# Performance work log

Measured on AMD Instinct MI355X. Metric: run time of the kernel, lower is better.

Reference implementation:

```python
import jax, jax.numpy as jnp
import numpy as np

D_IN = 1024
D_OUT = 1024
B = 4
S = 2048


def setup_inputs() -> dict:
    key = jax.random.key(0)
    kx, kq, kk, kv = jax.random.split(key, 4)
    x = jax.random.normal(kx, (B, S, D_IN), dtype=jnp.float32)
    # Linear weights stored as [d_in, d_out] so projection is x @ W
    sc = 1.0 / np.sqrt(D_IN)
    Wq = jax.random.normal(kq, (D_IN, D_OUT), dtype=jnp.float32) * sc
    Wk = jax.random.normal(kk, (D_IN, D_OUT), dtype=jnp.float32) * sc
    Wv = jax.random.normal(kv, (D_IN, D_OUT), dtype=jnp.float32) * sc
    return {"x": x, "Wq": Wq, "Wk": Wk, "Wv": Wv}


def reference(x, Wq, Wk, Wv):
    # q, k, v: [b, s, d_out]
    q = jnp.einsum("bsd,de->bse", x, Wq)
    k = jnp.einsum("bsd,de->bse", x, Wk)
    v = jnp.einsum("bsd,de->bse", x, Wv)
    s = q.shape[1]
    # raw scores [b, s, s]
    scores = jnp.einsum("bqd,bkd->bqk", q, k)
    # causal mask: disallow key j > query i (see notes re: original mask bug)
    causal = jnp.triu(jnp.ones((s, s), dtype=bool), k=1)
    scores = jnp.where(causal[None, :, :], -jnp.inf, scores)
    scale = 1.0 / jnp.sqrt(jnp.asarray(k.shape[-1], dtype=scores.dtype))
    att_weights = jax.nn.softmax(scores * scale, axis=-1)
    # dropout p=0.0 -> identity
    att_output = jnp.einsum("bqk,bkd->bqd", att_weights, v)
    return att_output, att_weights
```

## Files before the change

### kernel.cpp

```cpp
#include <hip/hip_runtime.h>
#include <stdint.h>

#define DIM 1024
#define SEQ 2048
#define NB 4

typedef unsigned short u16;
typedef __bf16 bf16x8 __attribute__((ext_vector_type(8)));
typedef float floatx4 __attribute__((ext_vector_type(4)));

__device__ __forceinline__ u16 f32_to_bf16(float f) {
  union { float f; unsigned u; } v; v.f = f;
  unsigned r = v.u + 0x7FFFu + ((v.u >> 16) & 1u);
  return (u16)(r >> 16);
}

__device__ __forceinline__ void async16(const void* g, void* l) {
  __builtin_amdgcn_global_load_lds(
      (__attribute__((address_space(1))) unsigned int*)g,
      (__attribute__((address_space(3))) unsigned int*)l, 16, 0, 0);
}

__global__ __launch_bounds__(256) void k_prep(const float* __restrict__ x,
                                              const float* __restrict__ Wq,
                                              const float* __restrict__ Wk,
                                              const float* __restrict__ Wv,
                                              u16* __restrict__ xb,
                                              u16* __restrict__ wt) {
  __shared__ u16 tile[32][33];
  const int bid = blockIdx.x;
  const int tid = threadIdx.x;
  if (bid < 4096) {
    int i = bid * 256 + tid;
    float4 a = ((const float4*)x)[i * 2];
    float4 b = ((const float4*)x)[i * 2 + 1];
    ushort4 o0, o1;
    o0.x = f32_to_bf16(a.x); o0.y = f32_to_bf16(a.y);
    o0.z = f32_to_bf16(a.z); o0.w = f32_to_bf16(a.w);
    o1.x = f32_to_bf16(b.x); o1.y = f32_to_bf16(b.y);
    o1.z = f32_to_bf16(b.z); o1.w = f32_to_bf16(b.w);
    ((ushort4*)xb)[i * 2] = o0;
    ((ushort4*)xb)[i * 2 + 1] = o1;
  } else {
    int t = bid - 4096;
    int z = t >> 10;
    int ti = t & 1023;
    int c0 = (ti & 31) * 32, r0 = (ti >> 5) * 32;
    const float* src = (z == 0) ? Wq : (z == 1) ? Wk : Wv;
    u16* d = wt + (size_t)z * DIM * DIM;
    int tx = tid & 31, ty = tid >> 5;
    #pragma unroll
    for (int dy = 0; dy < 32; dy += 8)
      tile[ty + dy][tx] = f32_to_bf16(src[(size_t)(r0 + ty + dy) * DIM + c0 + tx]);
    __syncthreads();
    #pragma unroll
    for (int dy = 0; dy < 32; dy += 8)
      d[(size_t)(c0 + ty + dy) * DIM + r0 + tx] = tile[tx][ty + dy];
  }
}


#define STG(PG, STBASE, SLOT, H, I, KT)                                        \
  async16((PG) + (size_t)((H) * 128 + (I) * 64) * DIM + (KT) * 64,             \
          (STBASE) + (SLOT) * 16384 + (H) * 8192 + (I) * 4096)

#define PHASE(SLOT, KS, MH, RDB, STGS, SYNC)                                   \
  {                                                                            \
    const int go_ = (KS) ? ga1 : ga0;                                          \
    const u16* pa_ = aRd + (SLOT) * 16384;                                     \
    if (RDB) {                                                                 \
      const u16* pb_ = bRd + (SLOT) * 16384;                                   \
      _Pragma("unroll") for (int n = 0; n < 4; ++n)                            \
          bfr[n] = *(const bf16x8*)(pb_ + n * 1024 + go_);                     \
    }                                                                          \
    _Pragma("unroll") for (int m = 0; m < 4; ++m)                              \
        af[m] = *(const bf16x8*)(pa_ + ((MH) * 4 + m) * 1024 + go_);           \
    STGS                                                                       \
    __builtin_amdgcn_s_barrier();                                              \
    asm volatile("s_waitcnt lgkmcnt(0)");                                      \
    __builtin_amdgcn_s_setprio(1);                                             \
    _Pragma("unroll") for (int m = 0; m < 4; ++m)                              \
        _Pragma("unroll") for (int n = 0; n < 4; ++n)                          \
            acc[(MH) * 4 + m][n] = __builtin_amdgcn_mfma_f32_16x16x32_bf16(    \
                af[m], bfr[n], acc[(MH) * 4 + m][n], 0, 0, 0);                 \
    __builtin_amdgcn_s_setprio(0);                                             \
    SYNC                                                                       \
    __builtin_amdgcn_s_barrier();                                              \
  }

__device__ __forceinline__ void core256(const u16* __restrict__ pga,
                                        const u16* __restrict__ pgb,
                                        const u16* aRd, const u16* bRd,
                                        u16* stA, u16* stB,
                                        int ga0, int ga1,
                                        floatx4 acc[8][4], int NITER) {
  bf16x8 af[4], bfr[4];

  STG(pga, stA, 0, 0, 0, 0); STG(pga, stA, 0, 0, 1, 0);
  STG(pga, stA, 0, 1, 0, 0); STG(pga, stA, 0, 1, 1, 0);
  STG(pgb, stB, 0, 0, 0, 0); STG(pgb, stB, 0, 0, 1, 0);
  STG(pgb, stB, 0, 1, 0, 0); STG(pgb, stB, 0, 1, 1, 0);
  STG(pgb, stB, 1, 0, 0, 1); STG(pgb, stB, 1, 0, 1, 1);
  asm volatile("s_waitcnt vmcnt(2)");
  __builtin_amdgcn_sched_barrier(0);
  __builtin_amdgcn_s_barrier();

  for (int t = 0; t < NITER; ++t) {
    const bool more = (t + 1 < NITER);
    const int kA1 = 2 * t + 1;
    const int kN = 2 * t + 2;
    const int kB1n = 2 * t + 3;

    PHASE(0, 0, 0, 1,
          { STG(pga, stA, 1, 0, 0, kA1); STG(pga, stA, 1, 0, 1, kA1); }, {})
    PHASE(0, 0, 1, 0,
          { STG(pga, stA, 1, 1, 0, kA1); STG(pga, stA, 1, 1, 1, kA1); }, {})
    PHASE(0, 1, 0, 1,
          { STG(pgb, stB, 1, 1, 0, kA1); STG(pgb, stB, 1, 1, 1, kA1); }, {})
    PHASE(0, 1, 1, 0,
          { if (more) { STG(pgb, stB, 0, 0, 0, kN); STG(pgb, stB, 0, 0, 1, kN); } },
          { if (more) { asm volatile("s_waitcnt vmcnt(2)"); }
            else      { asm volatile("s_waitcnt vmcnt(0)"); }
            __builtin_amdgcn_sched_barrier(0); })
    PHASE(1, 0, 0, 1,
          { if (more) { STG(pgb, stB, 0, 1, 0, kN); STG(pgb, stB, 0, 1, 1, kN); } }, {})
    PHASE(1, 0, 1, 0,
          { if (more) { STG(pga, stA, 0, 0, 0, kN); STG(pga, stA, 0, 0, 1, kN); } }, {})
    PHASE(1, 1, 0, 1,
          { if (more) { STG(pga, stA, 0, 1, 0, kN); STG(pga, stA, 0, 1, 1, kN); } }, {})
    PHASE(1, 1, 1, 0,
          { if (more) { STG(pgb, stB, 1, 0, 0, kB1n); STG(pgb, stB, 1, 0, 1, kB1n); } },
          { if (more) { asm volatile("s_waitcnt vmcnt(2)");
                        __builtin_amdgcn_sched_barrier(0); } })
  }

  asm volatile("s_waitcnt vmcnt(0)");
}

__global__ __launch_bounds__(512) void k_proj8(const u16* __restrict__ xb,
                                               const u16* __restrict__ wt,
                                               u16* __restrict__ qk,
                                               u16* __restrict__ vT) {
  __shared__ u16 lds[65536];
  const int wg = ((blockIdx.x & 7) * 48) + (blockIdx.x >> 3);
  const int tid = threadIdx.x;
  const int lane = tid & 63;
  const int wid = tid >> 6;

  const u16 *A, *Bt;
  u16* Cout;
  int ldc;
  if (wg < 256) {
    const int z = wg >> 7;
    const int r = wg & 127;
    const int mt = r >> 2, nt = r & 3;
    A = xb + (size_t)mt * 256 * DIM;
    Bt = wt + (size_t)z * DIM * DIM + (size_t)nt * 256 * DIM;
    Cout = qk + (size_t)z * (NB * SEQ * DIM) + (size_t)mt * 256 * DIM + nt * 256;
    ldc = DIM;
  } else {
    const int r = wg - 256;
    const int mt = r & 3, nt = r >> 2;
    A = wt + (size_t)2 * DIM * DIM + (size_t)mt * 256 * DIM;
    Bt = xb + (size_t)nt * 256 * DIM;
    Cout = vT + (size_t)(nt >> 3) * (DIM * SEQ) + (size_t)mt * 256 * SEQ
              + (nt & 7) * 256;
    ldc = SEQ;
  }

  const int srow = wid * 8 + (lane >> 3);
  const int gsrc = (lane & 7) ^ ((lane >> 3) & 7);
  const u16* pga = A + (size_t)srow * DIM + gsrc * 8;
  const u16* pgb = Bt + (size_t)srow * DIM + gsrc * 8;
  u16* stA = lds + wid * 512;
  u16* stB = lds + 32768 + wid * 512;

  const int wr = wid >> 2, wc = wid & 3;
  const int lrow = lane & 15, quad = lane >> 4;
  const int s = lrow & 7;
  const u16* aRd = lds + (wr * 128 + lrow) * 64;
  const u16* bRd = lds + 32768 + (wc * 64 + lrow) * 64;
  const int ga0 = (quad ^ s) << 3;
  const int ga1 = ga0 ^ 32;

  floatx4 acc[8][4] = {};
  core256(pga, pgb, aRd, bRd, stA, stB, ga0, ga1, acc, DIM / 128);

  u16* C = Cout + (size_t)(wr * 128 + quad * 4) * ldc + wc * 64 + lrow;
  #pragma unroll
  for (int m = 0; m < 8; ++m)
    #pragma unroll
    for (int rr = 0; rr < 4; ++rr)
      #pragma unroll
      for (int n = 0; n < 4; ++n)
        C[(size_t)(m * 16 + rr) * ldc + n * 16] = f32_to_bf16(acc[m][n][rr]);
}

__global__ __launch_bounds__(512) void k_scores(const u16* __restrict__ q,
                                                const u16* __restrict__ k,
                                                float* __restrict__ w) {
  __shared__ u16 lds[65536];
  const int wg = ((blockIdx.x & 7) * 18) + (blockIdx.x >> 3);
  const int b = wg / 36;
  const int t = wg % 36;
  int mt = (int)((sqrtf(8.0f * (float)t + 1.0f) - 1.0f) * 0.5f);
  while ((mt + 1) * (mt + 2) / 2 <= t) ++mt;
  while (mt * (mt + 1) / 2 > t) --mt;
  const int nt = t - mt * (mt + 1) / 2;

  const u16* A  = q + (size_t)b * SEQ * DIM + (size_t)mt * 256 * DIM;
  const u16* Bt = k + (size_t)b * SEQ * DIM + (size_t)nt * 256 * DIM;

  const int tid = threadIdx.x;
  const int lane = tid & 63;
  const int wid = tid >> 6;
  const int srow = wid * 8 + (lane >> 3);
  const int gsrc = (lane & 7) ^ ((lane >> 3) & 7);
  const u16* pga = A + (size_t)srow * DIM + gsrc * 8;
  const u16* pgb = Bt + (size_t)srow * DIM + gsrc * 8;
  u16* stA = lds + wid * 512;
  u16* stB = lds + 32768 + wid * 512;

  const int wr = wid >> 2, wc = wid & 3;
  const int lrow = lane & 15, quad = lane >> 4;
  const int s = lrow & 7;
  const u16* aRd = lds + (wr * 128 + lrow) * 64;
  const u16* bRd = lds + 32768 + (wc * 64 + lrow) * 64;
  const int ga0 = (quad ^ s) << 3;
  const int ga1 = ga0 ^ 32;

  floatx4 acc[8][4] = {};
  core256(pga, pgb, aRd, bRd, stA, stB, ga0, ga1, acc, DIM / 128);

  float* C = w + (size_t)b * SEQ * SEQ
               + (size_t)(mt * 256 + wr * 128 + quad * 4) * SEQ
               + nt * 256 + wc * 64 + lrow;
  #pragma unroll
  for (int m = 0; m < 8; ++m)
    #pragma unroll
    for (int rr = 0; rr < 4; ++rr)
      #pragma unroll
      for (int n = 0; n < 4; ++n)
        C[(size_t)(m * 16 + rr) * SEQ + n * 16] = acc[m][n][rr] * 0.03125f;
}

__device__ __forceinline__ void mfma_core128(const u16* __restrict__ A, int lda,
                                             const u16* __restrict__ Bt, int ldb,
                                             int kchunks, u16* lds,
                                             floatx4 acc[4][4]) {
  const int tid = threadIdx.x;
  const int lane = tid & 63;
  const int wid = tid >> 6;
  u16* lds_a = lds;
  u16* lds_b = lds + 16384;

  const int srow4 = lane >> 4;
  const int sgr = lane & 15;
  const int gbase = sgr ^ srow4;
  const u16* ag0 = A + (size_t)(wid * 32 + srow4) * lda + gbase * 8;
  const u16* ag1 = A + (size_t)(wid * 32 + srow4) * lda + (gbase ^ 4) * 8;
  const u16* bg0 = Bt + (size_t)(wid * 32 + srow4) * ldb + gbase * 8;
  const u16* bg1 = Bt + (size_t)(wid * 32 + srow4) * ldb + (gbase ^ 4) * 8;
  u16* la = lds_a + wid * 4096;
  u16* lb = lds_b + wid * 4096;

  const int wm = (wid >> 1) * 64, wn = (wid & 1) * 64;
  const int lrow = lane & 15, quad = lane >> 4;
  const int s = lrow & 7;
  const u16* pa = lds_a + (wm + lrow) * 128;
  const u16* pb = lds_b + (wn + lrow) * 128;

  for (int kt = 0; kt < kchunks; ++kt) {
    #pragma unroll
    for (int c = 0; c < 8; ++c) {
      const u16* sa = ((c & 1) ? ag1 : ag0) + (size_t)(c * 4) * lda;
      async16(sa, la + c * 512);
    }
    #pragma unroll
    for (int c = 0; c < 8; ++c) {
      const u16* sb = ((c & 1) ? bg1 : bg0) + (size_t)(c * 4) * ldb;
      async16(sb, lb + c * 512);
    }
    ag0 += 128; ag1 += 128; bg0 += 128; bg1 += 128;
    __syncthreads();
    #pragma unroll
    for (int ks = 0; ks < 4; ++ks) {
      const int g = (((ks << 2) | quad) ^ s) << 3;
      bf16x8 af[4], bfr[4];
      #pragma unroll
      for (int t = 0; t < 4; ++t) af[t] = *(const bf16x8*)(pa + t * 2048 + g);
      #pragma unroll
      for (int t = 0; t < 4; ++t) bfr[t] = *(const bf16x8*)(pb + t * 2048 + g);
      #pragma unroll
      for (int i = 0; i < 4; ++i)
        #pragma unroll
        for (int j = 0; j < 4; ++j)
          acc[i][j] = __builtin_amdgcn_mfma_f32_16x16x32_bf16(af[i], bfr[j],
                                                              acc[i][j], 0, 0, 0);
    }
    __syncthreads();
  }
}

__global__ __launch_bounds__(256) void k_softmax(float* __restrict__ w,
                                                 u16* __restrict__ P) {
  const int r = blockIdx.x;
  const int i = r & (SEQ - 1);
  const int len = i + 1;
  const int plen4 = (((i >> 7) + 1) << 7) >> 2;
  float4* srow = (float4*)(w + (size_t)r * SEQ);
  ushort4* prow = (ushort4*)(P + (size_t)r * SEQ);
  const int tid = threadIdx.x;
  const int lane = tid & 63, wid = tid >> 6;
  __shared__ float rm[4], rs[4];

  float4 e[2];
  float mx = -1e30f;
  #pragma unroll
  for (int u = 0; u < 2; ++u) {
    int q4 = tid + u * 256;
    int j0 = q4 * 4;
    float4 v = make_float4(-1e30f, -1e30f, -1e30f, -1e30f);
    if (j0 < len) {
      v = srow[q4];
      v.x = (j0 + 0 < len) ? v.x : -1e30f;
      v.y = (j0 + 1 < len) ? v.y : -1e30f;
      v.z = (j0 + 2 < len) ? v.z : -1e30f;
      v.w = (j0 + 3 < len) ? v.w : -1e30f;
    }
    e[u] = v;
    mx = fmaxf(mx, fmaxf(fmaxf(v.x, v.y), fmaxf(v.z, v.w)));
  }
  #pragma unroll
  for (int o = 32; o >= 1; o >>= 1) mx = fmaxf(mx, __shfl_xor(mx, o, 64));
  if (lane == 0) rm[wid] = mx;
  __syncthreads();
  mx = fmaxf(fmaxf(rm[0], rm[1]), fmaxf(rm[2], rm[3]));

  float sum = 0.f;
  #pragma unroll
  for (int u = 0; u < 2; ++u) {
    e[u].x = __expf(e[u].x - mx);
    e[u].y = __expf(e[u].y - mx);
    e[u].z = __expf(e[u].z - mx);
    e[u].w = __expf(e[u].w - mx);
    sum += e[u].x + e[u].y + e[u].z + e[u].w;
  }
  #pragma unroll
  for (int o = 32; o >= 1; o >>= 1) sum += __shfl_xor(sum, o, 64);
  if (lane == 0) rs[wid] = sum;
  __syncthreads();
  sum = rs[0] + rs[1] + rs[2] + rs[3];
  const float inv = 1.0f / sum;

  #pragma unroll
  for (int u = 0; u < 2; ++u) {
    int q4 = tid + u * 256;
    int j0 = q4 * 4;
    float4 v;
    v.x = (j0 + 0 < len) ? e[u].x * inv : 0.f;
    v.y = (j0 + 1 < len) ? e[u].y * inv : 0.f;
    v.z = (j0 + 2 < len) ? e[u].z * inv : 0.f;
    v.w = (j0 + 3 < len) ? e[u].w * inv : 0.f;
    srow[q4] = v;
    if (q4 < plen4) {
      ushort4 p;
      p.x = f32_to_bf16(v.x); p.y = f32_to_bf16(v.y);
      p.z = f32_to_bf16(v.z); p.w = f32_to_bf16(v.w);
      prow[q4] = p;
    }
  }
}

__global__ __launch_bounds__(256) void k_pv(const u16* __restrict__ P,
                                            const u16* __restrict__ vT,
                                            float* __restrict__ out) {
  const int id = blockIdx.x;
  const int mt = 15 - (id >> 5);
  const int nt = (id >> 2) & 7;
  const int b = id & 3;
  __shared__ u16 lds[32768];
  floatx4 acc[4][4] = {};
  mfma_core128(P + (size_t)b * SEQ * SEQ + (size_t)mt * 128 * SEQ, SEQ,
               vT + (size_t)b * DIM * SEQ + (size_t)nt * 128 * SEQ, SEQ,
               mt + 1, lds, acc);
  const int lane = threadIdx.x & 63, wid = threadIdx.x >> 6;
  const int wm = (wid >> 1) * 64, wn = (wid & 1) * 64;
  const int lrow = lane & 15, quad = lane >> 4;
  float* C = out + (size_t)b * SEQ * DIM
                 + (size_t)(mt * 128 + wm + quad * 4) * DIM + nt * 128 + wn + lrow;
  #pragma unroll
  for (int i = 0; i < 4; ++i)
    #pragma unroll
    for (int rr = 0; rr < 4; ++rr)
      #pragma unroll
      for (int j = 0; j < 4; ++j)
        C[(size_t)(i * 16 + rr) * DIM + j * 16] = acc[i][j][rr];
}

extern "C" void kernel_launch(void* const* d_in, const int* in_sizes, int n_in,
                              void* d_out, int out_size, void* d_ws, size_t ws_size,
                              hipStream_t stream) {
  const float* x  = (const float*)d_in[0];
  const float* Wq = (const float*)d_in[1];
  const float* Wk = (const float*)d_in[2];
  const float* Wv = (const float*)d_in[3];
  float* att_out = (float*)d_out;
  float* att_w   = (float*)d_out + 8388608;

  u16* xb = (u16*)d_ws;
  u16* wt = xb + 8388608;
  u16* qk = wt + 3145728;
  u16* vT = qk + 16777216;
  u16* P  = vT + 8388608;

  k_prep<<<7168, 256, 0, stream>>>(x, Wq, Wk, Wv, xb, wt);
  k_proj8<<<384, 512, 0, stream>>>(xb, wt, qk, vT);
  k_scores<<<144, 512, 0, stream>>>(qk, qk + 8388608, att_w);
  k_softmax<<<8192, 256, 0, stream>>>(att_w, P);
  k_pv<<<512, 256, 0, stream>>>(P, vT, att_out);
}
```

Measured before the change: 265.5 us.

## Zero upper-triangle score tiles in k_scores and split projection launch

Adds extra workgroups to k_scores that write zeros to the fully masked upper-triangle 256x256 tiles, and masks the diagonal tiles in the epilogue. The softmax kernel then only writes the causal prefix of each row instead of full rows. The aim is to shrink the wide fp32 writes in softmax and move the zero-fill into a kernel that has idle capacity at 144 blocks. The projection is also split into two launches of 192 blocks, which adds launch overhead and changes the block-to-XCD mapping.

```diff
diff --git a/kernel.cpp b/kernel.cpp
--- a/kernel.cpp
+++ b/kernel.cpp
@@ -140,9 +140,10 @@
 __global__ __launch_bounds__(512) void k_proj8(const u16* __restrict__ xb,
                                                const u16* __restrict__ wt,
                                                u16* __restrict__ qk,
-                                               u16* __restrict__ vT) {
+                                               u16* __restrict__ vT,
+                                               int base) {
   __shared__ u16 lds[65536];
-  const int wg = ((blockIdx.x & 7) * 48) + (blockIdx.x >> 3);
+  const int wg = ((blockIdx.x & 7) * 24) + (blockIdx.x >> 3) + base;
   const int tid = threadIdx.x;
   const int lane = tid & 63;
   const int wid = tid >> 6;
@@ -200,7 +201,26 @@
                                                 const u16* __restrict__ k,
                                                 float* __restrict__ w) {
   __shared__ u16 lds[65536];
-  const int wg = ((blockIdx.x & 7) * 18) + (blockIdx.x >> 3);
+  const int wg = ((blockIdx.x & 7) * 32) + (blockIdx.x >> 3);
+  const int tid = threadIdx.x;
+
+  if (wg >= 144) {
+    const int u = wg - 144;
+    const int b = u / 28;
+    int e = u % 28;
+    int mt = 0, acc0 = 0;
+    while (acc0 + (7 - mt) <= e) { acc0 += 7 - mt; ++mt; }
+    const int nt = mt + 1 + (e - acc0);
+    float4 z4 = make_float4(0.f, 0.f, 0.f, 0.f);
+    const int row = tid >> 1, half = tid & 1;
+    float4* p = (float4*)(w + (size_t)b * SEQ * SEQ
+                            + (size_t)(mt * 256 + row) * SEQ
+                            + nt * 256 + half * 128);
+    #pragma unroll
+    for (int kk = 0; kk < 32; ++kk) p[kk] = z4;
+    return;
+  }
+
   const int b = wg / 36;
   const int t = wg % 36;
   int mt = (int)((sqrtf(8.0f * (float)t + 1.0f) - 1.0f) * 0.5f);
@@ -211,7 +231,6 @@
   const u16* A  = q + (size_t)b * SEQ * DIM + (size_t)mt * 256 * DIM;
   const u16* Bt = k + (size_t)b * SEQ * DIM + (size_t)nt * 256 * DIM;
 
-  const int tid = threadIdx.x;
   const int lane = tid & 63;
   const int wid = tid >> 6;
   const int srow = wid * 8 + (lane >> 3);
@@ -232,16 +251,21 @@
   floatx4 acc[8][4] = {};
   core256(pga, pgb, aRd, bRd, stA, stB, ga0, ga1, acc, DIM / 128);
 
+  const bool diag = (mt == nt);
+  const int rb = wr * 128 + quad * 4;
+  const int cb = wc * 64 + lrow;
   float* C = w + (size_t)b * SEQ * SEQ
-               + (size_t)(mt * 256 + wr * 128 + quad * 4) * SEQ
-               + nt * 256 + wc * 64 + lrow;
+               + (size_t)(mt * 256 + rb) * SEQ + nt * 256 + cb;
   #pragma unroll
   for (int m = 0; m < 8; ++m)
     #pragma unroll
     for (int rr = 0; rr < 4; ++rr)
       #pragma unroll
-      for (int n = 0; n < 4; ++n)
-        C[(size_t)(m * 16 + rr) * SEQ + n * 16] = acc[m][n][rr] * 0.03125f;
+      for (int n = 0; n < 4; ++n) {
+        float val = acc[m][n][rr] * 0.03125f;
+        if (diag && (rb + m * 16 + rr) < (cb + n * 16)) val = 0.f;
+        C[(size_t)(m * 16 + rr) * SEQ + n * 16] = val;
+      }
 }
 
 __device__ __forceinline__ void mfma_core128(const u16* __restrict__ A, int lda,
@@ -357,13 +381,13 @@
   for (int u = 0; u < 2; ++u) {
     int q4 = tid + u * 256;
     int j0 = q4 * 4;
-    float4 v;
-    v.x = (j0 + 0 < len) ? e[u].x * inv : 0.f;
-    v.y = (j0 + 1 < len) ? e[u].y * inv : 0.f;
-    v.z = (j0 + 2 < len) ? e[u].z * inv : 0.f;
-    v.w = (j0 + 3 < len) ? e[u].w * inv : 0.f;
-    srow[q4] = v;
     if (q4 < plen4) {
+      float4 v;
+      v.x = (j0 + 0 < len) ? e[u].x * inv : 0.f;
+      v.y = (j0 + 1 < len) ? e[u].y * inv : 0.f;
+      v.z = (j0 + 2 < len) ? e[u].z * inv : 0.f;
+      v.w = (j0 + 3 < len) ? e[u].w * inv : 0.f;
+      srow[q4] = v;
       ushort4 p;
       p.x = f32_to_bf16(v.x); p.y = f32_to_bf16(v.y);
       p.z = f32_to_bf16(v.z); p.w = f32_to_bf16(v.w);
@@ -415,8 +439,9 @@
   u16* P  = vT + 8388608;
 
   k_prep<<<7168, 256, 0, stream>>>(x, Wq, Wk, Wv, xb, wt);
-  k_proj8<<<384, 512, 0, stream>>>(xb, wt, qk, vT);
-  k_scores<<<144, 512, 0, stream>>>(qk, qk + 8388608, att_w);
+  k_proj8<<<192, 512, 0, stream>>>(xb, wt, qk, vT, 0);
+  k_proj8<<<192, 512, 0, stream>>>(xb, wt, qk, vT, 192);
+  k_scores<<<256, 512, 0, stream>>>(qk, qk + 8388608, att_w);
   k_softmax<<<8192, 256, 0, stream>>>(att_w, P);
   k_pv<<<512, 256, 0, stream>>>(P, vT, att_out);
 }
```

Result: no change. 269.2 us (+1.4%).
